# Performance work log

Hardware: AMD Instinct MI355X
Metric: run time of the kernel (lower is better)

Reference implementation:

```python
import jax, jax.numpy as jnp
import numpy as np

N_NODES = 100000
N_EDGES = 1000000
IN_FEATS = 64
HID = 128
NUM_CLASSES = 10


def setup_inputs() -> dict:
    key = jax.random.key(0)
    ks = jax.random.split(key, 8)
    x = jax.random.normal(ks[0], (N_NODES, IN_FEATS), dtype=jnp.float32)
    edge_index = jax.random.randint(ks[1], (2, N_EDGES), 0, N_NODES, dtype=jnp.int64)
    # Glorot-style init scale for weights
    def w(k, fan_in, fan_out):
        s = (2.0 / (fan_in + fan_out)) ** 0.5
        return jax.random.normal(k, (fan_in, fan_out), dtype=jnp.float32) * s
    return {
        "x": x,
        "edge_index": edge_index,
        "W1": w(ks[2], IN_FEATS, HID),
        "b1": jnp.zeros((HID,), dtype=jnp.float32),
        "W2": w(ks[3], HID, HID),
        "b2": jnp.zeros((HID,), dtype=jnp.float32),
        "Wl": w(ks[4], HID, NUM_CLASSES),
        "bl": jnp.zeros((NUM_CLASSES,), dtype=jnp.float32),
    }


def _gcn_conv(x, src, dst, norm, W, b, num_nodes):
    # PyG GCNConv: h = x W, then out_i = sum_{j->i} norm_ij * h_j + b
    h = x @ W  # [N, out]
    msgs = h[src] * norm[:, None]  # gather + scale  [E+N, out]
    out = jax.ops.segment_sum(msgs, dst, num_segments=num_nodes)
    return out + b


def reference(x, edge_index, W1, b1, W2, b2, Wl, bl):
    N = x.shape[0]
    loops = jnp.arange(N, dtype=edge_index.dtype)
    src = jnp.concatenate([edge_index[0], loops])  # source nodes (messages from)
    dst = jnp.concatenate([edge_index[1], loops])  # target nodes (aggregate at)
    # symmetric normalization: deg over targets (includes self-loops)
    deg = jax.ops.segment_sum(jnp.ones(dst.shape, dtype=x.dtype), dst, num_segments=N)
    dinv = jnp.where(deg > 0, jax.lax.rsqrt(deg), 0.0)
    norm = dinv[src] * dinv[dst]  # [E+N]

    h = jax.nn.relu(_gcn_conv(x, src, dst, norm, W1, b1, N))
    h = jax.nn.relu(_gcn_conv(h, src, dst, norm, W2, b2, N))
    return jax.nn.log_softmax(h @ Wl + bl, axis=1)
```

## Files before the change

kernel.cpp:

```cpp
#include <hip/hip_runtime.h>
#include <hip/hip_fp16.h>
#include <math.h>

#define NUM_CLASSES 10

#define BSH 7
#define BSZ 128
#define BCAP 1792
#define NBMAX 1024
#define P1BATCH 4096
#define PREPB 97

typedef _Float16 half8  __attribute__((ext_vector_type(8)));
typedef _Float16 half4t __attribute__((ext_vector_type(4)));
typedef float    floatx4 __attribute__((ext_vector_type(4)));

__global__ __launch_bounds__(256) void prep_p1_kernel(const float* __restrict__ W1,
                                                      const float* __restrict__ W2,
                                                      const float* __restrict__ Wlc,
                                                      _Float16* __restrict__ W1t,
                                                      _Float16* __restrict__ W2t,
                                                      _Float16* __restrict__ Wct,
                                                      const int* __restrict__ src,
                                                      const int* __restrict__ dst,
                                                      int* __restrict__ bucket_fill,
                                                      unsigned* __restrict__ pairs, int E) {
    __shared__ int hist[NBMAX];
    __shared__ int lofs[NBMAX];
    __shared__ int gbase[NBMAX];
    __shared__ int cur[NBMAX];
    __shared__ int s1[256];
    __shared__ unsigned stage[P1BATCH];
    __shared__ unsigned short sbk[P1BATCH];
    const int tid = threadIdx.x;
    const int b = blockIdx.x;

    if (b < PREPB) {
        if (b < 32) {
            int i = b * 256 + tid;
            int k = i >> 7, c = i & 127;
            W1t[c * 72 + k] = (_Float16)W1[i];
        } else if (b < 96) {
            int i = (b - 32) * 256 + tid;
            int k = i >> 7, c = i & 127;
            W2t[c * 136 + k] = (_Float16)W2[i];
        } else {
            for (int i = tid; i < 16 * 136; i += 256) {
                int c = i / 136, k = i - c * 136;
                float v = (c < NUM_CLASSES && k < 128) ? Wlc[k * NUM_CLASSES + c] : 0.0f;
                Wct[i] = (_Float16)v;
            }
        }
        return;
    }

    const int blk = b - PREPB;
    for (int i = tid; i < NBMAX; i += 256) { hist[i] = 0; cur[i] = 0; }
    __syncthreads();

    const int bb = blk * P1BATCH;
    const int bcnt = min(P1BATCH, E - bb);
    unsigned pk[16];
    int bk[16];
    int cnt = 0;
#pragma unroll
    for (int i = 0; i < 16; ++i) {
        int idx = bb + i * 256 + tid;
        if (idx < E) {
            int s = src[idx], d = dst[idx];
            bk[i] = d >> BSH;
            pk[i] = ((unsigned)s << BSH) | (unsigned)(d & (BSZ - 1));
            atomicAdd(&hist[bk[i]], 1);
            cnt = i + 1;
        }
    }
    __syncthreads();
    const int i0 = tid * 4;
    int h4[4];
    int ssum = 0;
#pragma unroll
    for (int j = 0; j < 4; ++j) { h4[j] = hist[i0 + j]; ssum += h4[j]; }
    s1[tid] = ssum;
    __syncthreads();
    for (int off = 1; off < 256; off <<= 1) {
        int t = (tid >= off) ? s1[tid - off] : 0;
        __syncthreads();
        s1[tid] += t;
        __syncthreads();
    }
    int run = s1[tid] - ssum;
#pragma unroll
    for (int j = 0; j < 4; ++j) { lofs[i0 + j] = run; run += h4[j]; }
#pragma unroll
    for (int j = 0; j < 4; ++j)
        gbase[i0 + j] = (h4[j] > 0) ? atomicAdd(&bucket_fill[i0 + j], h4[j]) : 0;
    __syncthreads();
#pragma unroll
    for (int i = 0; i < 16; ++i) {
        if (i < cnt) {
            int bi = bk[i];
            int r = atomicAdd(&cur[bi], 1);
            int slot = lofs[bi] + r;
            stage[slot] = pk[i];
            sbk[slot] = (unsigned short)bi;
        }
    }
    __syncthreads();
    for (int j = tid; j < bcnt; j += 256) {
        int bi = sbk[j];
        int g = gbase[bi] + (j - lofs[bi]);
        if (g < BCAP) pairs[(size_t)bi * BCAP + g] = stage[j];
    }
}

__global__ __launch_bounds__(256) void csr_p2_kernel(const int* __restrict__ bucket_fill,
                                                     const unsigned* __restrict__ pairs,
                                                     const float* __restrict__ x,
                                                     int* __restrict__ rowstart,
                                                     float* __restrict__ dinv,
                                                     int* __restrict__ csr_src,
                                                     __half2* __restrict__ xs_h,
                                                     int N, int nbuck) {
    __shared__ int cnt[BSZ], excl[BSZ], cur[BSZ];
    __shared__ int s1[256];
    const int tid = threadIdx.x;
    const int b = blockIdx.x;
    const int node0 = b << BSH;
    const int nodes_b = min(BSZ, N - node0);

    if (tid < BSZ) { cnt[tid] = 0; cur[tid] = 0; }
    int part = 0;
    for (int j = tid; j < b; j += 256) part += bucket_fill[j];
    s1[tid] = part;
    __syncthreads();
    for (int off = 128; off > 0; off >>= 1) {
        if (tid < off) s1[tid] += s1[tid + off];
        __syncthreads();
    }
    const int bbase = s1[0];
    const int ne = bucket_fill[b];
    __syncthreads();

    const unsigned* bp = pairs + (size_t)b * BCAP;
    for (int i = tid; i < ne; i += 256)
        atomicAdd(&cnt[bp[i] & (BSZ - 1)], 1);
    __syncthreads();
    int c = (tid < BSZ) ? cnt[tid] : 0;
    if (tid < BSZ) s1[tid] = c;
    __syncthreads();
    for (int off = 1; off < BSZ; off <<= 1) {
        int t = (tid < BSZ && tid >= off) ? s1[tid - off] : 0;
        __syncthreads();
        if (tid < BSZ) s1[tid] += t;
        __syncthreads();
    }
    if (tid < BSZ) excl[tid] = s1[tid] - c;
    __syncthreads();

    if (tid < nodes_b) {
        rowstart[node0 + tid] = bbase + excl[tid];
        dinv[node0 + tid] = rsqrtf((float)cnt[tid] + 1.0f);
    }
    if (b == nbuck - 1 && tid == 0) rowstart[N] = bbase + ne;

    for (int i = tid; i < nodes_b * 32; i += 256) {
        int ln = i >> 5;
        float d = rsqrtf((float)cnt[ln] + 1.0f);
        float2 v = ((const float2*)x)[(size_t)node0 * 32 + i];
        xs_h[(size_t)node0 * 32 + i] = __floats2half2_rn(v.x * d, v.y * d);
    }
    for (int i = tid; i < ne; i += 256) {
        unsigned p = bp[i];
        int d = (int)(p & (BSZ - 1));
        int r = atomicAdd(&cur[d], 1);
        csr_src[bbase + excl[d] + r] = (int)(p >> BSH);
    }
}

__global__ __launch_bounds__(256) void gather64_kernel(const __half2* __restrict__ xs,
                                                       const float* __restrict__ dinv,
                                                       const int* __restrict__ rowstart,
                                                       const int* __restrict__ csr_src,
                                                       __half2* __restrict__ out, int N) {
    int node = (blockIdx.x * 256 + threadIdx.x) >> 6;
    int lane = threadIdx.x & 63;
    if (node >= N) return;
    const int h = lane >> 5;
    const int f2 = lane & 31;

    int beg = rowstart[node];
    int end = rowstart[node + 1];
    int deg = end - beg;

    float2 self = __half22float2(xs[(size_t)node * 32 + f2]);
    float2 acc = make_float2(0.f, 0.f);

    if (deg <= 16) {
        int myidx = (lane < deg) ? csr_src[beg + lane] : node;
        if (h == 0) {
            float cmp = (float)(deg - 15);
            acc.x = self.x * cmp;
            acc.y = self.y * cmp;
        }
        float2 v[8];
#pragma unroll
        for (int u = 0; u < 8; ++u) {
            int s = __shfl(myidx, 2 * u + h);
            v[u] = __half22float2(xs[(size_t)s * 32 + f2]);
        }
#pragma unroll
        for (int u = 0; u < 8; ++u) { acc.x += v[u].x; acc.y += v[u].y; }
    } else {
        int lim = deg < 64 ? deg : 64;
        int myidx = (lane < lim) ? csr_src[beg + lane] : node;
        int itersUp = (lim + 15) & ~15;
        if (h == 0) {
            float cmp = (float)(1 - (itersUp - lim));
            acc.x = self.x * cmp;
            acc.y = self.y * cmp;
        }
        for (int j = 0; j < itersUp; j += 16) {
            float2 v[8];
#pragma unroll
            for (int u = 0; u < 8; ++u) {
                int s = __shfl(myidx, j + 2 * u + h);
                v[u] = __half22float2(xs[(size_t)s * 32 + f2]);
            }
#pragma unroll
            for (int u = 0; u < 8; ++u) { acc.x += v[u].x; acc.y += v[u].y; }
        }
        if (h == 0) {
            for (int j = beg + 64; j < end; ++j) {
                float2 v = __half22float2(xs[(size_t)csr_src[j] * 32 + f2]);
                acc.x += v.x;
                acc.y += v.y;
            }
        }
    }
    acc.x += __shfl_xor(acc.x, 32);
    acc.y += __shfl_xor(acc.y, 32);
    if (lane < 32) {
        float d = dinv[node];
        out[(size_t)node * 32 + f2] = __floats2half2_rn(d * acc.x, d * acc.y);
    }
}

__global__ __launch_bounds__(256) void gather128_kernel(const __half2* __restrict__ hs,
                                                        const float* __restrict__ dinv,
                                                        const int* __restrict__ rowstart,
                                                        const int* __restrict__ csr_src,
                                                        __half2* __restrict__ out, int N) {
    int node = (blockIdx.x * 256 + threadIdx.x) >> 6;
    int lane = threadIdx.x & 63;
    if (node >= N) return;

    int beg = rowstart[node];
    int end = rowstart[node + 1];
    int deg = end - beg;

    float2 self = __half22float2(hs[(size_t)node * 64 + lane]);
    int lim = deg < 64 ? deg : 64;
    int myidx = (lane < lim) ? csr_src[beg + lane] : node;
    int itersUp = (lim + 7) & ~7;
    float comp = (float)(1 - (itersUp - lim));
    float2 acc;
    acc.x = self.x * comp;
    acc.y = self.y * comp;

    for (int j = 0; j < itersUp; j += 8) {
        int s[8];
#pragma unroll
        for (int u = 0; u < 8; ++u) s[u] = __shfl(myidx, j + u);
        float2 v[8];
#pragma unroll
        for (int u = 0; u < 8; ++u) v[u] = __half22float2(hs[(size_t)s[u] * 64 + lane]);
#pragma unroll
        for (int u = 0; u < 8; ++u) { acc.x += v[u].x; acc.y += v[u].y; }
    }
    for (int j = beg + 64; j < end; ++j) {
        float2 v = __half22float2(hs[(size_t)csr_src[j] * 64 + lane]);
        acc.x += v.x;
        acc.y += v.y;
    }
    float d = dinv[node];
    out[(size_t)node * 64 + lane] = __floats2half2_rn(d * acc.x, d * acc.y);
}

template <int K, bool SCALE_OUT>
__global__ __launch_bounds__(256) void gemm_mfma_kernel(const _Float16* __restrict__ In,
                                                        const _Float16* __restrict__ Wt,
                                                        const float* __restrict__ bias,
                                                        const float* __restrict__ dinv,
                                                        _Float16* __restrict__ Out, int N) {
    constexpr int KP = K + 8;
    constexpr int NC = K / 32;
    __shared__ _Float16 Wl[128 * KP];
    __shared__ float bias_s[128];
    const int tid = threadIdx.x;

    for (int i = tid; i < (128 * KP) / 8; i += 256)
        ((floatx4*)Wl)[i] = ((const floatx4*)Wt)[i];
    if (tid < 128) bias_s[tid] = bias[tid];
    __syncthreads();

    const int lane = tid & 63;
    const int wave = tid >> 6;
    const int q = lane >> 4;
    const int l15 = lane & 15;

#pragma unroll
    for (int iter = 0; iter < 2; ++iter) {
        int myrow = blockIdx.x * 128 + iter * 64 + wave * 16 + l15;
        int r = myrow < N ? myrow : N - 1;
        half8 xf[NC];
#pragma unroll
        for (int c = 0; c < NC; ++c)
            xf[c] = *(const half8*)(In + (size_t)r * K + c * 32 + q * 8);
        floatx4 acc[8];
#pragma unroll
        for (int t = 0; t < 8; ++t) acc[t] = (floatx4){0.f, 0.f, 0.f, 0.f};
#pragma unroll
        for (int c = 0; c < NC; ++c) {
#pragma unroll
            for (int t = 0; t < 8; ++t) {
                half8 wf = *(const half8*)(Wl + (t * 16 + l15) * KP + c * 32 + q * 8);
                acc[t] = __builtin_amdgcn_mfma_f32_16x16x32_f16(wf, xf[c], acc[t], 0, 0, 0);
            }
        }
        if (myrow < N) {
            float sc = SCALE_OUT ? dinv[myrow] : 1.0f;
#pragma unroll
            for (int t = 0; t < 8; ++t) {
                int c0 = t * 16 + q * 4;
                floatx4 bv = *(const floatx4*)&bias_s[c0];
                half4t hh;
#pragma unroll
                for (int j = 0; j < 4; ++j)
                    hh[j] = (_Float16)(sc * fmaxf(acc[t][j] + bv[j], 0.0f));
                *(half4t*)(Out + (size_t)myrow * 128 + c0) = hh;
            }
        }
    }
}

__global__ __launch_bounds__(256) void gemm_final_kernel(const _Float16* __restrict__ In,
                                                         const _Float16* __restrict__ Wt,
                                                         const float* __restrict__ bias,
                                                         const _Float16* __restrict__ Wct,
                                                         const float* __restrict__ bl,
                                                         float* __restrict__ out, int N) {
    constexpr int K = 128, KP = 136, NC = 4;
    __shared__ _Float16 Wl[128 * KP];
    __shared__ _Float16 Wc[16 * KP];
    __shared__ float bias_s[128];
    __shared__ float bl_s[16];
    __shared__ _Float16 act_s[4][16 * KP];
    const int tid = threadIdx.x;

    for (int i = tid; i < (128 * KP) / 8; i += 256)
        ((floatx4*)Wl)[i] = ((const floatx4*)Wt)[i];
    for (int i = tid; i < (16 * KP) / 8; i += 256)
        ((floatx4*)Wc)[i] = ((const floatx4*)Wct)[i];
    if (tid < 128) bias_s[tid] = bias[tid];
    if (tid < 16) bl_s[tid] = (tid < NUM_CLASSES) ? bl[tid] : -1e30f;
    __syncthreads();

    const int lane = tid & 63;
    const int wave = tid >> 6;
    const int q = lane >> 4;
    const int l15 = lane & 15;
    _Float16* As = act_s[wave];

    half8 wcf[NC];
#pragma unroll
    for (int c = 0; c < NC; ++c)
        wcf[c] = *(const half8*)(Wc + l15 * KP + c * 32 + q * 8);
    float myclsb[4];
#pragma unroll
    for (int reg = 0; reg < 4; ++reg) myclsb[reg] = bl_s[q * 4 + reg];

#pragma unroll
    for (int iter = 0; iter < 2; ++iter) {
        int myrow = blockIdx.x * 128 + iter * 64 + wave * 16 + l15;
        int r = myrow < N ? myrow : N - 1;
        half8 xf[NC];
#pragma unroll
        for (int c = 0; c < NC; ++c)
            xf[c] = *(const half8*)(In + (size_t)r * K + c * 32 + q * 8);
        floatx4 acc[8];
#pragma unroll
        for (int t = 0; t < 8; ++t) acc[t] = (floatx4){0.f, 0.f, 0.f, 0.f};
#pragma unroll
        for (int c = 0; c < NC; ++c) {
#pragma unroll
            for (int t = 0; t < 8; ++t) {
                half8 wf = *(const half8*)(Wl + (t * 16 + l15) * KP + c * 32 + q * 8);
                acc[t] = __builtin_amdgcn_mfma_f32_16x16x32_f16(wf, xf[c], acc[t], 0, 0, 0);
            }
        }
#pragma unroll
        for (int t = 0; t < 8; ++t) {
            int c0 = t * 16 + q * 4;
            floatx4 bv = *(const floatx4*)&bias_s[c0];
            half4t hh;
#pragma unroll
            for (int j = 0; j < 4; ++j)
                hh[j] = (_Float16)fmaxf(acc[t][j] + bv[j], 0.0f);
            *(half4t*)&As[l15 * KP + c0] = hh;
        }
        floatx4 lg = (floatx4){0.f, 0.f, 0.f, 0.f};
#pragma unroll
        for (int c = 0; c < NC; ++c) {
            half8 af = *(const half8*)(As + l15 * KP + c * 32 + q * 8);
            lg = __builtin_amdgcn_mfma_f32_16x16x32_f16(wcf[c], af, lg, 0, 0, 0);
        }
        if (myrow < N) {
            float v[4];
#pragma unroll
            for (int reg = 0; reg < 4; ++reg) v[reg] = lg[reg] + myclsb[reg];
            float mx = fmaxf(fmaxf(v[0], v[1]), fmaxf(v[2], v[3]));
            mx = fmaxf(mx, __shfl_xor(mx, 16));
            mx = fmaxf(mx, __shfl_xor(mx, 32));
            float sm = expf(v[0] - mx) + expf(v[1] - mx) + expf(v[2] - mx) + expf(v[3] - mx);
            sm += __shfl_xor(sm, 16);
            sm += __shfl_xor(sm, 32);
            float lse = mx + logf(sm);
#pragma unroll
            for (int reg = 0; reg < 4; ++reg) {
                int cls = q * 4 + reg;
                if (cls < NUM_CLASSES)
                    out[(size_t)myrow * NUM_CLASSES + cls] = v[reg] - lse;
            }
        }
    }
}

extern "C" void kernel_launch(void* const* d_in, const int* in_sizes, int n_in,
                              void* d_out, int out_size, void* d_ws, size_t ws_size,
                              hipStream_t stream) {
    const float* x  = (const float*)d_in[0];
    const int*   ei = (const int*)d_in[1];
    const float* W1 = (const float*)d_in[2];
    const float* b1 = (const float*)d_in[3];
    const float* W2 = (const float*)d_in[4];
    const float* b2 = (const float*)d_in[5];
    const float* Wlc = (const float*)d_in[6];
    const float* bl = (const float*)d_in[7];
    float* out = (float*)d_out;

    const int N = in_sizes[0] / 64;
    const int E = in_sizes[1] / 2;
    const int* src = ei;
    const int* dst = ei + E;
    const int nbuck = (N + BSZ - 1) >> BSH;

    char* ws = (char*)d_ws;
    int*      bucket_fill = (int*)(ws + 0);
    int*      rowstart    = (int*)(ws + 4096);
    float*    dinv        = (float*)(ws + 524288);
    _Float16* W1t         = (_Float16*)(ws + 1048576);
    _Float16* W2t         = (_Float16*)(ws + 1069056);
    _Float16* Wct         = (_Float16*)(ws + 1103872);
    unsigned* pairs       = (unsigned*)(ws + 2097152);
    int*      csr_src     = (int*)(ws + 12582912);
    __half2*  xs_h        = (__half2*)(ws + 16777216);
    __half2*  g1h         = (__half2*)(ws + 33554432);
    __half2*  g2h         = (__half2*)(ws + 46923776);
    __half2*  a1_h        = (__half2*)(ws + 73400320);

    const int P1B = (E + P1BATCH - 1) / P1BATCH;
    const int GB  = (N + 127) / 128;
    const int WVB = (N + 3) / 4;

    hipMemsetAsync(bucket_fill, 0, nbuck * sizeof(int), stream);
    prep_p1_kernel<<<PREPB + P1B, 256, 0, stream>>>(W1, W2, Wlc, W1t, W2t, Wct,
                                                    src, dst, bucket_fill, pairs, E);
    csr_p2_kernel<<<nbuck, 256, 0, stream>>>(bucket_fill, pairs, x, rowstart, dinv,
                                             csr_src, xs_h, N, nbuck);

    gather64_kernel<<<WVB, 256, 0, stream>>>(xs_h, dinv, rowstart, csr_src, g1h, N);
    gemm_mfma_kernel<64, true><<<GB, 256, 0, stream>>>((const _Float16*)g1h, W1t, b1, dinv,
                                                       (_Float16*)a1_h, N);

    gather128_kernel<<<WVB, 256, 0, stream>>>(a1_h, dinv, rowstart, csr_src, g2h, N);
    gemm_final_kernel<<<GB, 256, 0, stream>>>((const _Float16*)g2h, W2t, b2, Wct, bl, out, N);
}
```

Before: 233.0 us.

## Split prep from CSR pass, simplify bucket scatter, and halve-split layer-2 gather

Weight transposition and bucket_fill zeroing move into a separate prep kernel, which replaces the memset and the merged launch. The CSR pass-1 kernel drops the LDS staging, prefix scan and coalesced write-out and scatters pairs to global memory directly through atomic slot offsets. The 128-wide layer-2 gather is split into two launches, each covering 64 features, with the two half-waves handling alternate neighbors and combined by a shuffle. The aim is fewer barriers and less LDS in pass 1 and a smaller per-launch gather footprint, at the cost of uncoalesced pair writes, an extra launch, and re-reading the CSR indices twice.

```diff
diff --git a/kernel.cpp b/kernel.cpp
--- a/kernel.cpp
+++ b/kernel.cpp
@@ -9,57 +9,48 @@
 #define BCAP 1792
 #define NBMAX 1024
 #define P1BATCH 4096
-#define PREPB 97
 
 typedef _Float16 half8  __attribute__((ext_vector_type(8)));
 typedef _Float16 half4t __attribute__((ext_vector_type(4)));
 typedef float    floatx4 __attribute__((ext_vector_type(4)));
 
-__global__ __launch_bounds__(256) void prep_p1_kernel(const float* __restrict__ W1,
-                                                      const float* __restrict__ W2,
-                                                      const float* __restrict__ Wlc,
-                                                      _Float16* __restrict__ W1t,
-                                                      _Float16* __restrict__ W2t,
-                                                      _Float16* __restrict__ Wct,
-                                                      const int* __restrict__ src,
-                                                      const int* __restrict__ dst,
-                                                      int* __restrict__ bucket_fill,
-                                                      unsigned* __restrict__ pairs, int E) {
-    __shared__ int hist[NBMAX];
-    __shared__ int lofs[NBMAX];
-    __shared__ int gbase[NBMAX];
-    __shared__ int cur[NBMAX];
-    __shared__ int s1[256];
-    __shared__ unsigned stage[P1BATCH];
-    __shared__ unsigned short sbk[P1BATCH];
+__global__ __launch_bounds__(256) void prep_kernel(const float* __restrict__ W1,
+                                                   const float* __restrict__ W2,
+                                                   const float* __restrict__ Wlc,
+                                                   _Float16* __restrict__ W1t,
+                                                   _Float16* __restrict__ W2t,
+                                                   _Float16* __restrict__ Wct,
+                                                   int* __restrict__ fill, int nbuck) {
+    const int b = blockIdx.x, tid = threadIdx.x;
+    if (b == 0) {
+        for (int i = tid; i < nbuck; i += 256) fill[i] = 0;
+    }
+    if (b < 32) {
+        int i = b * 256 + tid;
+        int k = i >> 7, c = i & 127;
+        W1t[c * 72 + k] = (_Float16)W1[i];
+    } else if (b < 96) {
+        int i = (b - 32) * 256 + tid;
+        int k = i >> 7, c = i & 127;
+        W2t[c * 136 + k] = (_Float16)W2[i];
+    } else {
+        for (int i = tid; i < 16 * 136; i += 256) {
+            int c = i / 136, k = i - c * 136;
+            float v = (c < NUM_CLASSES && k < 128) ? Wlc[k * NUM_CLASSES + c] : 0.0f;
+            Wct[i] = (_Float16)v;
+        }
+    }
+}
+
+__global__ __launch_bounds__(256) void csr_p1_kernel(const int* __restrict__ src,
+                                                     const int* __restrict__ dst,
+                                                     int* __restrict__ bucket_fill,
+                                                     unsigned* __restrict__ pairs, int E) {
+    __shared__ int hist[NBMAX], base[NBMAX], cur[NBMAX];
     const int tid = threadIdx.x;
-    const int b = blockIdx.x;
-
-    if (b < PREPB) {
-        if (b < 32) {
-            int i = b * 256 + tid;
-            int k = i >> 7, c = i & 127;
-            W1t[c * 72 + k] = (_Float16)W1[i];
-        } else if (b < 96) {
-            int i = (b - 32) * 256 + tid;
-            int k = i >> 7, c = i & 127;
-            W2t[c * 136 + k] = (_Float16)W2[i];
-        } else {
-            for (int i = tid; i < 16 * 136; i += 256) {
-                int c = i / 136, k = i - c * 136;
-                float v = (c < NUM_CLASSES && k < 128) ? Wlc[k * NUM_CLASSES + c] : 0.0f;
-                Wct[i] = (_Float16)v;
-            }
-        }
-        return;
-    }
-
-    const int blk = b - PREPB;
     for (int i = tid; i < NBMAX; i += 256) { hist[i] = 0; cur[i] = 0; }
     __syncthreads();
-
-    const int bb = blk * P1BATCH;
-    const int bcnt = min(P1BATCH, E - bb);
+    const int bb = blockIdx.x * P1BATCH;
     unsigned pk[16];
     int bk[16];
     int cnt = 0;
@@ -75,41 +66,16 @@
         }
     }
     __syncthreads();
-    const int i0 = tid * 4;
-    int h4[4];
-    int ssum = 0;
-#pragma unroll
-    for (int j = 0; j < 4; ++j) { h4[j] = hist[i0 + j]; ssum += h4[j]; }
-    s1[tid] = ssum;
-    __syncthreads();
-    for (int off = 1; off < 256; off <<= 1) {
-        int t = (tid >= off) ? s1[tid - off] : 0;
-        __syncthreads();
-        s1[tid] += t;
-        __syncthreads();
-    }
-    int run = s1[tid] - ssum;
-#pragma unroll
-    for (int j = 0; j < 4; ++j) { lofs[i0 + j] = run; run += h4[j]; }
-#pragma unroll
-    for (int j = 0; j < 4; ++j)
-        gbase[i0 + j] = (h4[j] > 0) ? atomicAdd(&bucket_fill[i0 + j], h4[j]) : 0;
+    for (int i = tid; i < NBMAX; i += 256)
+        if (hist[i] > 0) base[i] = atomicAdd(&bucket_fill[i], hist[i]);
     __syncthreads();
 #pragma unroll
     for (int i = 0; i < 16; ++i) {
         if (i < cnt) {
-            int bi = bk[i];
-            int r = atomicAdd(&cur[bi], 1);
-            int slot = lofs[bi] + r;
-            stage[slot] = pk[i];
-            sbk[slot] = (unsigned short)bi;
-        }
-    }
-    __syncthreads();
-    for (int j = tid; j < bcnt; j += 256) {
-        int bi = sbk[j];
-        int g = gbase[bi] + (j - lofs[bi]);
-        if (g < BCAP) pairs[(size_t)bi * BCAP + g] = stage[j];
+            int b = bk[i];
+            int r = atomicAdd(&cur[b], 1) + base[b];
+            if (r < BCAP) pairs[(size_t)b * BCAP + r] = pk[i];
+        }
     }
 }
 
@@ -245,45 +211,73 @@
     }
 }
 
-__global__ __launch_bounds__(256) void gather128_kernel(const __half2* __restrict__ hs,
-                                                        const float* __restrict__ dinv,
-                                                        const int* __restrict__ rowstart,
-                                                        const int* __restrict__ csr_src,
-                                                        __half2* __restrict__ out, int N) {
+__global__ __launch_bounds__(256) void gather128h_kernel(const __half2* __restrict__ hs,
+                                                         const float* __restrict__ dinv,
+                                                         const int* __restrict__ rowstart,
+                                                         const int* __restrict__ csr_src,
+                                                         __half2* __restrict__ out,
+                                                         int N, int hofs) {
     int node = (blockIdx.x * 256 + threadIdx.x) >> 6;
     int lane = threadIdx.x & 63;
     if (node >= N) return;
+    const int h = lane >> 5;
+    const int f2 = (lane & 31) + hofs;
 
     int beg = rowstart[node];
     int end = rowstart[node + 1];
     int deg = end - beg;
 
-    float2 self = __half22float2(hs[(size_t)node * 64 + lane]);
-    int lim = deg < 64 ? deg : 64;
-    int myidx = (lane < lim) ? csr_src[beg + lane] : node;
-    int itersUp = (lim + 7) & ~7;
-    float comp = (float)(1 - (itersUp - lim));
-    float2 acc;
-    acc.x = self.x * comp;
-    acc.y = self.y * comp;
-
-    for (int j = 0; j < itersUp; j += 8) {
-        int s[8];
-#pragma unroll
-        for (int u = 0; u < 8; ++u) s[u] = __shfl(myidx, j + u);
+    float2 self = __half22float2(hs[(size_t)node * 64 + f2]);
+    float2 acc = make_float2(0.f, 0.f);
+
+    if (deg <= 16) {
+        int myidx = (lane < deg) ? csr_src[beg + lane] : node;
+        if (h == 0) {
+            float cmp = (float)(deg - 15);
+            acc.x = self.x * cmp;
+            acc.y = self.y * cmp;
+        }
         float2 v[8];
 #pragma unroll
-        for (int u = 0; u < 8; ++u) v[u] = __half22float2(hs[(size_t)s[u] * 64 + lane]);
+        for (int u = 0; u < 8; ++u) {
+            int s = __shfl(myidx, 2 * u + h);
+            v[u] = __half22float2(hs[(size_t)s * 64 + f2]);
+        }
 #pragma unroll
         for (int u = 0; u < 8; ++u) { acc.x += v[u].x; acc.y += v[u].y; }
-    }
-    for (int j = beg + 64; j < end; ++j) {
-        float2 v = __half22float2(hs[(size_t)csr_src[j] * 64 + lane]);
-        acc.x += v.x;
-        acc.y += v.y;
-    }
-    float d = dinv[node];
-    out[(size_t)node * 64 + lane] = __floats2half2_rn(d * acc.x, d * acc.y);
+    } else {
+        int lim = deg < 64 ? deg : 64;
+        int myidx = (lane < lim) ? csr_src[beg + lane] : node;
+        int itersUp = (lim + 15) & ~15;
+        if (h == 0) {
+            float cmp = (float)(1 - (itersUp - lim));
+            acc.x = self.x * cmp;
+            acc.y = self.y * cmp;
+        }
+        for (int j = 0; j < itersUp; j += 16) {
+            float2 v[8];
+#pragma unroll
+            for (int u = 0; u < 8; ++u) {
+                int s = __shfl(myidx, j + 2 * u + h);
+                v[u] = __half22float2(hs[(size_t)s * 64 + f2]);
+            }
+#pragma unroll
+            for (int u = 0; u < 8; ++u) { acc.x += v[u].x; acc.y += v[u].y; }
+        }
+        if (h == 0) {
+            for (int j = beg + 64; j < end; ++j) {
+                float2 v = __half22float2(hs[(size_t)csr_src[j] * 64 + f2]);
+                acc.x += v.x;
+                acc.y += v.y;
+            }
+        }
+    }
+    acc.x += __shfl_xor(acc.x, 32);
+    acc.y += __shfl_xor(acc.y, 32);
+    if (lane < 32) {
+        float d = dinv[node];
+        out[(size_t)node * 64 + f2] = __floats2half2_rn(d * acc.x, d * acc.y);
+    }
 }
 
 template <int K, bool SCALE_OUT>
@@ -472,9 +466,8 @@
     const int GB  = (N + 127) / 128;
     const int WVB = (N + 3) / 4;
 
-    hipMemsetAsync(bucket_fill, 0, nbuck * sizeof(int), stream);
-    prep_p1_kernel<<<PREPB + P1B, 256, 0, stream>>>(W1, W2, Wlc, W1t, W2t, Wct,
-                                                    src, dst, bucket_fill, pairs, E);
+    prep_kernel<<<97, 256, 0, stream>>>(W1, W2, Wlc, W1t, W2t, Wct, bucket_fill, nbuck);
+    csr_p1_kernel<<<P1B, 256, 0, stream>>>(src, dst, bucket_fill, pairs, E);
     csr_p2_kernel<<<nbuck, 256, 0, stream>>>(bucket_fill, pairs, x, rowstart, dinv,
                                              csr_src, xs_h, N, nbuck);
 
@@ -482,6 +475,7 @@
     gemm_mfma_kernel<64, true><<<GB, 256, 0, stream>>>((const _Float16*)g1h, W1t, b1, dinv,
                                                        (_Float16*)a1_h, N);
 
-    gather128_kernel<<<WVB, 256, 0, stream>>>(a1_h, dinv, rowstart, csr_src, g2h, N);
+    gather128h_kernel<<<WVB, 256, 0, stream>>>(a1_h, dinv, rowstart, csr_src, g2h, N, 0);
+    gather128h_kernel<<<WVB, 256, 0, stream>>>(a1_h, dinv, rowstart, csr_src, g2h, N, 32);
     gemm_final_kernel<<<GB, 256, 0, stream>>>((const _Float16*)g2h, W2t, b2, Wct, bl, out, N);
 }
```

Result: no change. 234.9 us (+0.8%).
